# Optimization experiments

Measured on AMD Instinct MI355X. Metric: run time of the kernel, lower is better.

## Reference

```python
import jax, jax.numpy as jnp
import numpy as np

D_MODEL = 2048
N_HEADS = 16
D_HEAD = D_MODEL // N_HEADS
BATCH = 4
SEQ = 2048


def setup_inputs() -> dict:
    key = jax.random.key(0)
    ks = jax.random.split(key, 10)
    s = 1.0 / np.sqrt(D_MODEL)
    inp = {
        "x": jax.random.normal(ks[0], (BATCH, SEQ, D_MODEL), dtype=jnp.float32),
        "attn_mask": jnp.ones((1, 1, SEQ, SEQ), dtype=jnp.int32),
        "Wq": jax.random.uniform(ks[1], (D_MODEL, D_MODEL), jnp.float32, -s, s),
        "bq": jax.random.uniform(ks[2], (D_MODEL,), jnp.float32, -s, s),
        "Wk": jax.random.uniform(ks[3], (D_MODEL, D_MODEL), jnp.float32, -s, s),
        "bk": jax.random.uniform(ks[4], (D_MODEL,), jnp.float32, -s, s),
        "Wv": jax.random.uniform(ks[5], (D_MODEL, D_MODEL), jnp.float32, -s, s),
        "bv": jax.random.uniform(ks[6], (D_MODEL,), jnp.float32, -s, s),
        "Wo": jax.random.uniform(ks[7], (D_MODEL, D_MODEL), jnp.float32, -s, s),
        "bo": jax.random.uniform(ks[8], (D_MODEL,), jnp.float32, -s, s),
    }
    return inp


def reference(x, attn_mask, Wq, bq, Wk, bk, Wv, bv, Wo, bo):
    B, S, D = x.shape
    # projections (torch Linear: x @ W.T + b); split heads -> (B, H, S, Dh)
    def split(t):
        return t.reshape(B, S, N_HEADS, D_HEAD).transpose(0, 2, 1, 3)
    q = split(x @ Wq.T + bq)
    k = split(x @ Wk.T + bk)
    v = split(x @ Wv.T + bv)
    scale = 1.0 / np.sqrt(D_HEAD).astype(np.float32)
    scores = jnp.einsum('bhqd,bhkd->bhqk', q, k) * scale  # (B,H,S,S)
    scores = jnp.where(attn_mask == 0, jnp.float32(-jnp.inf), scores)
    attn = jax.nn.softmax(scores, axis=-1)
    out = jnp.einsum('bhqk,bhkd->bhqd', attn, v)  # (B,H,S,Dh)
    out = out.transpose(0, 2, 1, 3).reshape(B, S, D)
    return out @ Wo.T + bo
```

## Files before the change

### kernel.cpp

```cpp
#include <hip/hip_runtime.h>
#include <stdint.h>
#include <stddef.h>

typedef __attribute__((ext_vector_type(8))) short short8;
typedef __attribute__((ext_vector_type(4))) float f32x4;

#define SEQ    2048
#define DMODEL 2048
#define NHEAD  16
#define DHEAD  128
#define BATCH  4
#define KVT    32
#define NKVT   (SEQ / KVT)

__device__ __forceinline__ unsigned short f2b(float f) {
  unsigned int u;
  __builtin_memcpy(&u, &f, sizeof(u));
  u = u + 0x7FFFu + ((u >> 16) & 1u);
  return (unsigned short)(u >> 16);
}

__device__ __forceinline__ void gload16(const void* g, void* l) {
  __builtin_amdgcn_global_load_lds(
      (const __attribute__((address_space(1))) unsigned int*)g,
      (__attribute__((address_space(3))) unsigned int*)l, 16, 0, 0);
}


__global__ __launch_bounds__(256) void cvt_x_kernel(
    const float* __restrict__ src, unsigned short* __restrict__ dst, int n8)
{
  const int idx = blockIdx.x * 256 + threadIdx.x;
  if (idx >= n8) return;
  const f32x4 a = *(const f32x4*)(src + (size_t)idx * 8);
  const f32x4 b = *(const f32x4*)(src + (size_t)idx * 8 + 4);
  short8 o;
  o[0] = (short)f2b(a[0]); o[1] = (short)f2b(a[1]);
  o[2] = (short)f2b(a[2]); o[3] = (short)f2b(a[3]);
  o[4] = (short)f2b(b[0]); o[5] = (short)f2b(b[1]);
  o[6] = (short)f2b(b[2]); o[7] = (short)f2b(b[3]);
  const int i = idx >> 8;
  const int k = (idx & 255) * 8;
  const size_t e = ((size_t)(i >> 4) * 64 + (k >> 5)) * 512
                 + (((k >> 3) & 3) * 16 + (i & 15)) * 8;
  *(short8*)(dst + e) = o;
}

__global__ __launch_bounds__(256) void cvt_w_kernel(
    const float* __restrict__ s0, const float* __restrict__ s1,
    const float* __restrict__ s2, const float* __restrict__ s3,
    unsigned short* __restrict__ dst, int n8)
{
  const int y = blockIdx.y;
  const float* src = (y == 0) ? s0 : (y == 1) ? s1 : (y == 2) ? s2 : s3;
  unsigned short* d = dst + (size_t)y * DMODEL * DMODEL;
  const int idx = blockIdx.x * 256 + threadIdx.x;
  if (idx >= n8) return;
  const f32x4 a = *(const f32x4*)(src + (size_t)idx * 8);
  const f32x4 b = *(const f32x4*)(src + (size_t)idx * 8 + 4);
  short8 o;
  o[0] = (short)f2b(a[0]); o[1] = (short)f2b(a[1]);
  o[2] = (short)f2b(a[2]); o[3] = (short)f2b(a[3]);
  o[4] = (short)f2b(b[0]); o[5] = (short)f2b(b[1]);
  o[6] = (short)f2b(b[2]); o[7] = (short)f2b(b[3]);
  const int i = idx >> 8;
  const int k = (idx & 255) * 8;
  const size_t e = ((size_t)(i >> 4) * 64 + (k >> 5)) * 512
                 + (((k >> 3) & 3) * 16 + (i & 15)) * 8;
  *(short8*)(d + e) = o;
}

__global__ __launch_bounds__(512, 2) void gemm_bt_kernel(
    const unsigned short* __restrict__ A,
    const unsigned short* __restrict__ W0, const unsigned short* __restrict__ W1,
    const unsigned short* __restrict__ W2,
    const float* __restrict__ b0, const float* __restrict__ b1,
    const float* __restrict__ b2,
    unsigned short* __restrict__ o0, unsigned short* __restrict__ o1,
    unsigned short* __restrict__ o2,
    float* __restrict__ of,
    int mode_base)
{
  const int z = blockIdx.z;
  const unsigned short* W    = (z == 0) ? W0 : (z == 1) ? W1 : W2;
  const float* bias          = (z == 0) ? b0 : (z == 1) ? b1 : b2;
  unsigned short* out        = (z == 0) ? o0 : (z == 1) ? o1 : o2;
  const int mode = mode_base + z;

  const int m0 = blockIdx.y * 256;
  const int n0 = blockIdx.x * 256;

  __shared__ __align__(16) unsigned short LA[4][8192];
  __shared__ __align__(16) unsigned short LB[4][8192];

  const int tid = threadIdx.x;
  const int wid = tid >> 6;
  const int ln  = tid & 63;
  const int l15 = ln & 15;
  const int lg  = ln >> 4;
  const int wr  = wid >> 2;
  const int wc  = wid & 3;

  const int arow = m0 >> 4;
  const int brow = n0 >> 4;

  auto stageA = [&](int kt) {
    const unsigned short* s = A + ((size_t)(arow + wid) * 64 + kt) * 512 + ln * 8;
    unsigned short* d = &LA[kt & 3][wid * 512 + ln * 8];
    gload16(s, d);
    gload16(s + (size_t)8 * 64 * 512, d + 8 * 512);
  };
  auto stageB = [&](int kt) {
    const unsigned short* s = W + ((size_t)(brow + wid) * 64 + kt) * 512 + ln * 8;
    unsigned short* d = &LB[kt & 3][wid * 512 + ln * 8];
    gload16(s, d);
    gload16(s + (size_t)8 * 64 * 512, d + 8 * 512);
  };

  f32x4 acc[8][4];
#pragma unroll
  for (int m = 0; m < 8; ++m)
#pragma unroll
    for (int n = 0; n < 4; ++n) acc[m][n] = (f32x4){0.f, 0.f, 0.f, 0.f};

  stageA(0); stageB(0); stageA(1); stageB(1); stageA(2); stageB(2);
  asm volatile("s_waitcnt vmcnt(8)" ::: "memory");
  __builtin_amdgcn_s_barrier();

  for (int j = 0; j < 64; ++j) {
    const int buf = j & 3;

    short8 a[8], bA[2];
#pragma unroll
    for (int mi = 0; mi < 8; ++mi)
      a[mi] = *(const short8*)(&LA[buf][(wr * 8 + mi) * 512 + ln * 8]);
#pragma unroll
    for (int ni = 0; ni < 2; ++ni)
      bA[ni] = *(const short8*)(&LB[buf][(wc * 4 + ni) * 512 + ln * 8]);
    if (j + 3 < 64) stageA(j + 3);
    __builtin_amdgcn_s_barrier();
    asm volatile("s_waitcnt lgkmcnt(0)" ::: "memory");
    __builtin_amdgcn_sched_barrier(0);
    __builtin_amdgcn_s_setprio(1);
#pragma unroll
    for (int mi = 0; mi < 8; ++mi)
#pragma unroll
      for (int ni = 0; ni < 2; ++ni)
        acc[mi][ni] = __builtin_amdgcn_mfma_f32_16x16x32_bf16(a[mi], bA[ni], acc[mi][ni], 0, 0, 0);
    __builtin_amdgcn_s_setprio(0);
    __builtin_amdgcn_s_barrier();

    short8 bB[2];
#pragma unroll
    for (int ni = 0; ni < 2; ++ni)
      bB[ni] = *(const short8*)(&LB[buf][(wc * 4 + 2 + ni) * 512 + ln * 8]);
    if (j + 3 < 64) stageB(j + 3);
    __builtin_amdgcn_s_barrier();
    asm volatile("s_waitcnt lgkmcnt(0)" ::: "memory");
    __builtin_amdgcn_sched_barrier(0);
    __builtin_amdgcn_s_setprio(1);
#pragma unroll
    for (int mi = 0; mi < 8; ++mi)
#pragma unroll
      for (int ni = 0; ni < 2; ++ni)
        acc[mi][2 + ni] = __builtin_amdgcn_mfma_f32_16x16x32_bf16(a[mi], bB[ni], acc[mi][2 + ni], 0, 0, 0);
    __builtin_amdgcn_s_setprio(0);
    if (j <= 60)      asm volatile("s_waitcnt vmcnt(8)" ::: "memory");
    else if (j == 61) asm volatile("s_waitcnt vmcnt(4)" ::: "memory");
    else if (j == 62) asm volatile("s_waitcnt vmcnt(0)" ::: "memory");
    __builtin_amdgcn_s_barrier();
  }

#pragma unroll
  for (int n = 0; n < 4; ++n) {
    const int jj = n0 + wc * 64 + n * 16 + l15;
    const float bb = bias[jj];
#pragma unroll
    for (int m = 0; m < 8; ++m) {
#pragma unroll
      for (int r = 0; r < 4; ++r) {
        const int i = m0 + wr * 128 + m * 16 + lg * 4 + r;
        float v = acc[m][n][r] + bb;
        if (mode == 0) v *= 0.0883883476483184f;
        if (mode == 3) {
          of[(size_t)i * DMODEL + jj] = v;
        } else {
          const int b = i >> 11, s = i & 2047, hh = jj >> 7, dh = jj & 127;
          const size_t bhOff = (size_t)(b * 16 + hh) * (SEQ * DHEAD);
          size_t addr;
          if (mode == 0)
            addr = bhOff + (size_t)s * DHEAD + dh;
          else if (mode == 1)
            addr = bhOff + (size_t)(s >> 4) * 2048 + (dh >> 5) * 512
                 + ((dh >> 3) & 3) * 128 + (s & 15) * 8 + (dh & 7);
          else
            addr = bhOff + (size_t)(s >> 5) * 4096 + (dh >> 4) * 512
                 + ((s >> 3) & 3) * 128 + (dh & 15) * 8 + (s & 7);
          out[addr] = f2b(v);
        }
      }
    }
  }
}

__global__ __launch_bounds__(256, 4) void attn_kernel(
    const unsigned short* __restrict__ Q,
    const unsigned short* __restrict__ Kf,
    const unsigned short* __restrict__ Vf,
    unsigned short* __restrict__ AO)
{
  const int idx = blockIdx.x;
  const int xcd = idx & 7;
  const int sq  = idx >> 3;
  const int bh  = xcd * 8 + (sq >> 5);
  const int qt  = sq & 31;

  const int wave = threadIdx.x >> 6;
  const int lane = threadIdx.x & 63;
  const int l15  = lane & 15;
  const int lg   = lane >> 4;
  const int q0   = qt * 64 + wave * 16;

  const unsigned short* Qb = Q  + (size_t)bh * SEQ * DHEAD;
  const unsigned short* Kb = Kf + (size_t)bh * SEQ * DHEAD;
  const unsigned short* Vb = Vf + (size_t)bh * SEQ * DHEAD;

  __shared__ __align__(16) unsigned short Ks[2][4096];
  __shared__ __align__(16) unsigned short Vs[2][4096];
  __shared__ __align__(16) unsigned short P[4][16][40];

  short8 qf[4];
#pragma unroll
  for (int k = 0; k < 4; ++k)
    qf[k] = *(const short8*)(Qb + (size_t)(q0 + l15) * DHEAD + k * 32 + lg * 8);

  short8 onesf;
#pragma unroll
  for (int e = 0; e < 8; ++e) onesf[e] = (short)0x3F80;

  f32x4 oacc[9];
#pragma unroll
  for (int n = 0; n < 9; ++n) oacc[n] = (f32x4){0.f, 0.f, 0.f, 0.f};
  float mrun[4];
#pragma unroll
  for (int r = 0; r < 4; ++r) mrun[r] = -1e30f;

  const int t = threadIdx.x;
  auto STAGE = [&](int buf, int kvt) {
    const unsigned short* ksrc = Kb + (size_t)kvt * 4096;
    const unsigned short* vsrc = Vb + (size_t)kvt * 4096;
    gload16(ksrc + t * 8,        &Ks[buf][t * 8]);
    gload16(ksrc + 2048 + t * 8, &Ks[buf][2048 + t * 8]);
    gload16(vsrc + t * 8,        &Vs[buf][t * 8]);
    gload16(vsrc + 2048 + t * 8, &Vs[buf][2048 + t * 8]);
  };

  STAGE(0, 0);

  for (int kvt = 0; kvt < NKVT; ++kvt) {
    const int cur = kvt & 1;
    if (kvt + 1 < NKVT) {
      STAGE(cur ^ 1, kvt + 1);
      asm volatile("s_waitcnt vmcnt(4)" ::: "memory");
    } else {
      asm volatile("s_waitcnt vmcnt(0)" ::: "memory");
    }
    __builtin_amdgcn_s_barrier();
    __builtin_amdgcn_sched_barrier(0);

    f32x4 sacc[2];
#pragma unroll
    for (int n = 0; n < 2; ++n) sacc[n] = (f32x4){0.f, 0.f, 0.f, 0.f};
    __builtin_amdgcn_s_setprio(1);
#pragma unroll
    for (int n = 0; n < 2; ++n) {
#pragma unroll
      for (int k = 0; k < 4; ++k) {
        short8 kfr = *(const short8*)(&Ks[cur][n * 2048 + k * 512 + lane * 8]);
        sacc[n] = __builtin_amdgcn_mfma_f32_16x16x32_bf16(qf[k], kfr, sacc[n], 0, 0, 0);
      }
    }
    __builtin_amdgcn_s_setprio(0);

    float d = -1e30f;
#pragma unroll
    for (int r = 0; r < 4; ++r)
      d = fmaxf(d, fmaxf(sacc[0][r], sacc[1][r]) - mrun[r]);
    if (__any(d > 8.f)) {
#pragma unroll
      for (int r = 0; r < 4; ++r) {
        float m = fmaxf(sacc[0][r], sacc[1][r]);
        m = fmaxf(m, __shfl_xor(m, 1));
        m = fmaxf(m, __shfl_xor(m, 2));
        m = fmaxf(m, __shfl_xor(m, 4));
        m = fmaxf(m, __shfl_xor(m, 8));
        if (m > mrun[r]) {
          const float alpha = __expf(mrun[r] - m);
#pragma unroll
          for (int n = 0; n < 9; ++n) oacc[n][r] *= alpha;
          mrun[r] = m;
        }
      }
    }

#pragma unroll
    for (int n = 0; n < 2; ++n)
#pragma unroll
      for (int r = 0; r < 4; ++r)
        P[wave][lg * 4 + r][n * 16 + l15] =
            (unsigned short)f2b(__expf(sacc[n][r] - mrun[r]));
    asm volatile("s_waitcnt lgkmcnt(0)" ::: "memory");
    __builtin_amdgcn_sched_barrier(0);

    short8 pf = *(const short8*)(&P[wave][l15][lg * 8]);
    __builtin_amdgcn_s_setprio(1);
#pragma unroll
    for (int n = 0; n < 8; ++n) {
      short8 vfr = *(const short8*)(&Vs[cur][n * 512 + lane * 8]);
      oacc[n] = __builtin_amdgcn_mfma_f32_16x16x32_bf16(pf, vfr, oacc[n], 0, 0, 0);
    }
    oacc[8] = __builtin_amdgcn_mfma_f32_16x16x32_bf16(pf, onesf, oacc[8], 0, 0, 0);
    __builtin_amdgcn_s_setprio(0);

    asm volatile("s_waitcnt lgkmcnt(0)" ::: "memory");
    __builtin_amdgcn_s_barrier();
    __builtin_amdgcn_sched_barrier(0);
  }

  const int b = bh >> 4, h = bh & 15;
  float inv[4];
#pragma unroll
  for (int r = 0; r < 4; ++r) inv[r] = 1.f / oacc[8][r];
#pragma unroll
  for (int n = 0; n < 8; ++n) {
    const int kk  = h * 4 + (n >> 1);
    const int sub = (n * 2 + (l15 >> 3)) & 3;
#pragma unroll
    for (int r = 0; r < 4; ++r) {
      const int i = b * SEQ + q0 + lg * 4 + r;
      const size_t e = ((size_t)(i >> 4) * 64 + kk) * 512
                     + sub * 128 + (i & 15) * 8 + (l15 & 7);
      AO[e] = f2b(oacc[n][r] * inv[r]);
    }
  }
}

extern "C" void kernel_launch(void* const* d_in, const int* in_sizes, int n_in,
                              void* d_out, int out_size, void* d_ws, size_t ws_size,
                              hipStream_t stream)
{
  const float* xf  = (const float*)d_in[0];
  const float* Wqf = (const float*)d_in[2];
  const float* bq  = (const float*)d_in[3];
  const float* Wkf = (const float*)d_in[4];
  const float* bk  = (const float*)d_in[5];
  const float* Wvf = (const float*)d_in[6];
  const float* bv  = (const float*)d_in[7];
  const float* Wof = (const float*)d_in[8];
  const float* bo  = (const float*)d_in[9];
  float* out = (float*)d_out;

  const size_t QE = (size_t)64 * SEQ * DHEAD;
  const size_t WE = (size_t)DMODEL * DMODEL;

  unsigned short* Qw = (unsigned short*)d_out;
  unsigned short* Kw = Qw + QE;

  unsigned short* Vtw = (unsigned short*)d_ws;
  unsigned short* AOw = Vtw + QE;
  unsigned short* xb  = AOw + QE;
  unsigned short* Wb  = xb + QE;
  unsigned short* Wqb = Wb;
  unsigned short* Wkb = Wb + WE;
  unsigned short* Wvb = Wb + 2 * WE;
  unsigned short* Wob = Wb + 3 * WE;

  cvt_x_kernel<<<dim3((int)(QE / 8 / 256)), 256, 0, stream>>>(xf, xb, (int)(QE / 8));
  cvt_w_kernel<<<dim3((int)(WE / 8 / 256), 4), 256, 0, stream>>>(
      Wqf, Wkf, Wvf, Wof, Wb, (int)(WE / 8));

  gemm_bt_kernel<<<dim3(8, 32, 3), 512, 0, stream>>>(
      xb, Wqb, Wkb, Wvb, bq, bk, bv, Qw, Kw, Vtw, nullptr, 0);

  attn_kernel<<<dim3(2048), 256, 0, stream>>>(Qw, Kw, Vtw, AOw);

  gemm_bt_kernel<<<dim3(8, 32, 1), 512, 0, stream>>>(
      AOw, Wob, Wob, Wob, bo, bo, bo, nullptr, nullptr, nullptr, out, 3);
}
```

Measured before the change: 571.1 us.

## Restructure GEMM mainloop with register-prefetched A fragments and single barrier

The projection GEMM mainloop is reorganized into one barrier per k-step. A and B staging are merged into a single call, all four B fragments are issued at once, and the next step's A fragments are prefetched from LDS into registers while the current MFMAs run. Block indices are also remapped so that four consecutive M tiles share an N tile, which should improve L2 reuse of weights. The change aims to cut barrier and LDS-latency stalls, at the cost of extra VGPRs for the double-buffered A fragments. That could pressure occupancy under the 512x2 launch bound.

```diff
diff --git a/kernel.cpp b/kernel.cpp
--- a/kernel.cpp
+++ b/kernel.cpp
@@ -87,8 +87,10 @@
   unsigned short* out        = (z == 0) ? o0 : (z == 1) ? o1 : o2;
   const int mode = mode_base + z;
 
-  const int m0 = blockIdx.y * 256;
-  const int n0 = blockIdx.x * 256;
+  const int mt = blockIdx.x * 4 + (blockIdx.y & 3);
+  const int nt = blockIdx.y >> 2;
+  const int m0 = mt * 256;
+  const int n0 = nt * 256;
 
   __shared__ __align__(16) unsigned short LA[4][8192];
   __shared__ __align__(16) unsigned short LB[4][8192];
@@ -101,21 +103,18 @@
   const int wr  = wid >> 2;
   const int wc  = wid & 3;
 
-  const int arow = m0 >> 4;
-  const int brow = n0 >> 4;
-
-  auto stageA = [&](int kt) {
-    const unsigned short* s = A + ((size_t)(arow + wid) * 64 + kt) * 512 + ln * 8;
-    unsigned short* d = &LA[kt & 3][wid * 512 + ln * 8];
-    gload16(s, d);
-    gload16(s + (size_t)8 * 64 * 512, d + 8 * 512);
+  const unsigned short* sA = A + ((size_t)((m0 >> 4) + wid) * 64) * 512 + ln * 8;
+  const unsigned short* sB = W + ((size_t)((n0 >> 4) + wid) * 64) * 512 + ln * 8;
+  const size_t FROW8 = (size_t)8 * 64 * 512;
+
+  auto stage = [&](int kt) {
+    unsigned short* dA = &LA[kt & 3][wid * 512 + ln * 8];
+    unsigned short* dB = &LB[kt & 3][wid * 512 + ln * 8];
+    gload16(sA + (size_t)kt * 512,         dA);
+    gload16(sA + FROW8 + (size_t)kt * 512, dA + 8 * 512);
+    gload16(sB + (size_t)kt * 512,         dB);
+    gload16(sB + FROW8 + (size_t)kt * 512, dB + 8 * 512);
   };
-  auto stageB = [&](int kt) {
-    const unsigned short* s = W + ((size_t)(brow + wid) * 64 + kt) * 512 + ln * 8;
-    unsigned short* d = &LB[kt & 3][wid * 512 + ln * 8];
-    gload16(s, d);
-    gload16(s + (size_t)8 * 64 * 512, d + 8 * 512);
-  };
 
   f32x4 acc[8][4];
 #pragma unroll
@@ -123,52 +122,46 @@
 #pragma unroll
     for (int n = 0; n < 4; ++n) acc[m][n] = (f32x4){0.f, 0.f, 0.f, 0.f};
 
-  stageA(0); stageB(0); stageA(1); stageB(1); stageA(2); stageB(2);
+  stage(0); stage(1); stage(2);
   asm volatile("s_waitcnt vmcnt(8)" ::: "memory");
   __builtin_amdgcn_s_barrier();
 
+  short8 aCur[8], aNxt[8], bCur[4];
+#pragma unroll
+  for (int mi = 0; mi < 8; ++mi)
+    aCur[mi] = *(const short8*)(&LA[0][(wr * 8 + mi) * 512 + ln * 8]);
+
+#pragma unroll 2
   for (int j = 0; j < 64; ++j) {
     const int buf = j & 3;
-
-    short8 a[8], bA[2];
-#pragma unroll
-    for (int mi = 0; mi < 8; ++mi)
-      a[mi] = *(const short8*)(&LA[buf][(wr * 8 + mi) * 512 + ln * 8]);
-#pragma unroll
-    for (int ni = 0; ni < 2; ++ni)
-      bA[ni] = *(const short8*)(&LB[buf][(wc * 4 + ni) * 512 + ln * 8]);
-    if (j + 3 < 64) stageA(j + 3);
+    if (j <= 61)      asm volatile("s_waitcnt vmcnt(4)" ::: "memory");
+    else if (j == 62) asm volatile("s_waitcnt vmcnt(0)" ::: "memory");
     __builtin_amdgcn_s_barrier();
-    asm volatile("s_waitcnt lgkmcnt(0)" ::: "memory");
+    if (j + 3 < 64) stage(j + 3);
+#pragma unroll
+    for (int ni = 0; ni < 4; ++ni)
+      bCur[ni] = *(const short8*)(&LB[buf][(wc * 4 + ni) * 512 + ln * 8]);
+    if (j < 63) {
+      const int nbuf = (j + 1) & 3;
+#pragma unroll
+      for (int mi = 0; mi < 8; ++mi)
+        aNxt[mi] = *(const short8*)(&LA[nbuf][(wr * 8 + mi) * 512 + ln * 8]);
+      __builtin_amdgcn_sched_barrier(0);
+      asm volatile("s_waitcnt lgkmcnt(8)" ::: "memory");
+    } else {
+      __builtin_amdgcn_sched_barrier(0);
+      asm volatile("s_waitcnt lgkmcnt(0)" ::: "memory");
+    }
     __builtin_amdgcn_sched_barrier(0);
     __builtin_amdgcn_s_setprio(1);
 #pragma unroll
     for (int mi = 0; mi < 8; ++mi)
 #pragma unroll
-      for (int ni = 0; ni < 2; ++ni)
-        acc[mi][ni] = __builtin_amdgcn_mfma_f32_16x16x32_bf16(a[mi], bA[ni], acc[mi][ni], 0, 0, 0);
+      for (int ni = 0; ni < 4; ++ni)
+        acc[mi][ni] = __builtin_amdgcn_mfma_f32_16x16x32_bf16(aCur[mi], bCur[ni], acc[mi][ni], 0, 0, 0);
     __builtin_amdgcn_s_setprio(0);
-    __builtin_amdgcn_s_barrier();
-
-    short8 bB[2];
-#pragma unroll
-    for (int ni = 0; ni < 2; ++ni)
-      bB[ni] = *(const short8*)(&LB[buf][(wc * 4 + 2 + ni) * 512 + ln * 8]);
-    if (j + 3 < 64) stageB(j + 3);
-    __builtin_amdgcn_s_barrier();
-    asm volatile("s_waitcnt lgkmcnt(0)" ::: "memory");
-    __builtin_amdgcn_sched_barrier(0);
-    __builtin_amdgcn_s_setprio(1);
-#pragma unroll
-    for (int mi = 0; mi < 8; ++mi)
-#pragma unroll
-      for (int ni = 0; ni < 2; ++ni)
-        acc[mi][2 + ni] = __builtin_amdgcn_mfma_f32_16x16x32_bf16(a[mi], bB[ni], acc[mi][2 + ni], 0, 0, 0);
-    __builtin_amdgcn_s_setprio(0);
-    if (j <= 60)      asm volatile("s_waitcnt vmcnt(8)" ::: "memory");
-    else if (j == 61) asm volatile("s_waitcnt vmcnt(4)" ::: "memory");
-    else if (j == 62) asm volatile("s_waitcnt vmcnt(0)" ::: "memory");
-    __builtin_amdgcn_s_barrier();
+#pragma unroll
+    for (int mi = 0; mi < 8; ++mi) aCur[mi] = aNxt[mi];
   }
 
 #pragma unroll
```

After: 616.0 us. 7.9% more time.
